# Kernel optimization log

Measured on AMD Instinct MI355X. Metric: run time of the kernel, lower is better.

Reference implementation:

```python
import jax, jax.numpy as jnp
import numpy as np
from functools import partial

B, S, V, E, H = 32, 48, 32000, 512, 512


def setup_inputs() -> dict:
    key = jax.random.key(0)
    ks = jax.random.split(key, 8)
    s = 0.02
    return {
        "encoded": jax.random.normal(ks[0], (B, E), jnp.float32),
        "emb": jax.random.normal(ks[1], (V, E), jnp.float32) * s,   # embedding table
        "Wi": jax.random.normal(ks[2], (4 * H, E), jnp.float32) * s,  # input->gates
        "Wh": jax.random.normal(ks[3], (4 * H, H), jnp.float32) * s,  # hidden->gates
        "bi": jnp.zeros((4 * H,), jnp.float32),
        "bh": jnp.zeros((4 * H,), jnp.float32),
        "Wo": jax.random.normal(ks[4], (V, H), jnp.float32) * s,   # hidden->vocab logits
        "bo": jnp.zeros((V,), jnp.float32),
        "seq_length": S,
    }


def reference(encoded, emb, Wi, Wh, bi, bh, Wo, bo, seq_length):
    """Batched autoregressive decode (teacher_forcing=False path).

    Each step: LSTM cell -> log_softmax over vocab -> store (if still active)
    -> multinomial sample -> embed sampled token as next input. Early EOS
    (token == V-2) is handled by masking stored log-probs to zero thereafter,
    matching the original loop that leaves probs rows as zeros after break.
    """
    bsz = encoded.shape[0]
    hid = Wh.shape[1]
    vocab = Wo.shape[0]
    bias = bi + bh

    def step(carry, k):
        x, h, c, active = carry
        gates = x @ Wi.T + h @ Wh.T + bias          # [B, 4H]
        i_g, f_g, g_g, o_g = jnp.split(gates, 4, axis=-1)  # torch gate order i,f,g,o
        i_g = jax.nn.sigmoid(i_g)
        f_g = jax.nn.sigmoid(f_g)
        g_g = jnp.tanh(g_g)
        o_g = jax.nn.sigmoid(o_g)
        c = f_g * c + i_g * g_g
        h = o_g * jnp.tanh(c)
        logp = jax.nn.log_softmax(h @ Wo.T + bo, axis=-1)  # [B, V]
        stored = jnp.where(active[:, None], logp, 0.0)
        it = jax.random.categorical(k, logp, axis=-1)      # multinomial(exp(logp))
        active = active & (it != vocab - 2)                # EOS token check
        x = emb[it]                                        # next-step input
        return (x, h, c, active), stored

    keys = jax.random.split(jax.random.key(42), seq_length)
    init = (encoded,
            jnp.zeros((bsz, hid), encoded.dtype),
            jnp.zeros((bsz, hid), encoded.dtype),
            jnp.ones((bsz,), bool))
    _, probs = jax.lax.scan(step, init, keys)              # [S, B, V]
    return jnp.transpose(probs, (1, 0, 2))                 # [B, S, V]
```

## Files before the change

### kernel.cpp

```cpp
#include <hip/hip_runtime.h>
#include <stdint.h>
#include <math.h>
#include <limits.h>


#define SEQ 48
#define BSZ 32
#define VOC 32000
#define EDIM 512
#define HDIM 512
#define GDIM 2048
#define KTOT 1024
#define EOS_TOK (VOC - 2)
#define NBLK 250

typedef __attribute__((ext_vector_type(8))) short bf16x8;
typedef __attribute__((ext_vector_type(4))) float f32x4;

__device__ __forceinline__ void threefry2x32(uint32_t k0, uint32_t k1,
                                             uint32_t x0, uint32_t x1,
                                             uint32_t& o0, uint32_t& o1)
{
  uint32_t ks2 = k0 ^ k1 ^ 0x1BD11BDAu;
  x0 += k0; x1 += k1;
#define TFR(r) x0 += x1; x1 = (x1 << (r)) | (x1 >> (32 - (r))); x1 ^= x0;
  TFR(13) TFR(15) TFR(26) TFR(6)
  x0 += k1; x1 += ks2 + 1u;
  TFR(17) TFR(29) TFR(16) TFR(24)
  x0 += ks2; x1 += k0 + 2u;
  TFR(13) TFR(15) TFR(26) TFR(6)
  x0 += k0; x1 += k1 + 3u;
  TFR(17) TFR(29) TFR(16) TFR(24)
  x0 += k1; x1 += ks2 + 4u;
  TFR(13) TFR(15) TFR(26) TFR(6)
  x0 += ks2; x1 += k0 + 5u;
#undef TFR
  o0 = x0; o1 = x1;
}

__device__ __forceinline__ uint32_t tf_bits(uint32_t k0, uint32_t k1, uint32_t m)
{
  uint32_t o0, o1;
  threefry2x32(k0, k1, 0u, m, o0, o1);
  return o0 ^ o1;
}

__device__ __forceinline__ float gumbel_from_bits(uint32_t bits)
{
  uint32_t fb = (bits >> 9) | 0x3F800000u;
  float u = __uint_as_float(fb) - 1.0f;
  u = fmaxf(u, 1.1754943508222875e-38f);
  return -logf(-logf(u));
}

__device__ __forceinline__ float sigmoidf(float v) { return 1.0f / (1.0f + expf(-v)); }

__device__ __forceinline__ unsigned short f2bf(float f) {
  uint32_t u = __float_as_uint(f);
  uint32_t r = u + 0x7FFFu + ((u >> 16) & 1u);
  return (unsigned short)(r >> 16);
}
__device__ __forceinline__ float bf2f(unsigned short h) {
  return __uint_as_float((uint32_t)h << 16);
}

__device__ __forceinline__ float dlf(const float* p) {
  return __hip_atomic_load(p, __ATOMIC_RELAXED, __HIP_MEMORY_SCOPE_AGENT);
}
__device__ __forceinline__ int dli(const int* p) {
  return __hip_atomic_load(p, __ATOMIC_RELAXED, __HIP_MEMORY_SCOPE_AGENT);
}
__device__ __forceinline__ void dsf(float* p, float v) {
  __hip_atomic_store(p, v, __ATOMIC_RELAXED, __HIP_MEMORY_SCOPE_AGENT);
}
__device__ __forceinline__ void dsi(int* p, int v) {
  __hip_atomic_store(p, v, __ATOMIC_RELAXED, __HIP_MEMORY_SCOPE_AGENT);
}

__global__ __launch_bounds__(256) void init_kernel(
    const float* __restrict__ encoded, float* __restrict__ h0,
    float* __restrict__ c, float* __restrict__ x,
    int* __restrict__ active, uint32_t* __restrict__ keys,
    int* __restrict__ counter)
{
  int i = blockIdx.x * 256 + threadIdx.x;
  if (i < BSZ * HDIM) { h0[i] = 0.0f; c[i] = 0.0f; x[i] = encoded[i]; }
  if (blockIdx.x == 0) {
    int t = threadIdx.x;
    if (t < BSZ) active[t] = 1;
    if (t < SEQ) {
      counter[t] = 0;
      uint32_t o0, o1;
      threefry2x32(0u, 42u, 0u, (uint32_t)t, o0, o1);
      keys[2 * t] = o0; keys[2 * t + 1] = o1;
    }
  }
}

__global__ void transpose_kernel(const float* __restrict__ src, float* __restrict__ dst,
                                 int R, int C, int dstLD, int cOff)
{
  __shared__ float tile[32][33];
  int cb = blockIdx.x * 32, rb = blockIdx.y * 32;
  int tx = threadIdx.x, ty = threadIdx.y;
  for (int j = ty; j < 32; j += 8) {
    int r = rb + j, cc = cb + tx;
    if (r < R && cc < C) tile[j][tx] = src[(size_t)r * C + cc];
  }
  __syncthreads();
  for (int j = ty; j < 32; j += 8) {
    int r = rb + tx, cc = cb + j;
    if (r < R && cc < C) dst[(size_t)(cc + cOff) * dstLD + r] = tile[tx][j];
  }
}

__global__ __launch_bounds__(256) void wprep_kernel(
    const float* __restrict__ Wo, unsigned short* __restrict__ WP)
{
  int i4 = blockIdx.x * 256 + threadIdx.x;
  if (i4 >= VOC * 128) return;
  int v  = i4 >> 7;
  int k  = (i4 & 127) * 4;
  const float4 wv = ((const float4*)Wo)[i4];
  int bid  = v >> 7;
  int nt   = (v >> 4) & 7;
  int lane = (v & 15) + (((k >> 3) & 3) << 4);
  int ks   = k >> 5;
  int e0   = k & 7;
  size_t f = (((size_t)bid * 16 + ks) * 8 + nt) * 2;
  size_t base = f * 512 + (size_t)lane * 8 + e0;
  unsigned short a0 = f2bf(wv.x), a1 = f2bf(wv.y), a2 = f2bf(wv.z), a3 = f2bf(wv.w);
  *(ushort4*)(WP + base)       = make_ushort4(a0, a1, a2, a3);
  *(ushort4*)(WP + base + 512) = make_ushort4(f2bf(wv.x - bf2f(a0)), f2bf(wv.y - bf2f(a1)),
                                              f2bf(wv.z - bf2f(a2)), f2bf(wv.w - bf2f(a3)));
}

__global__ __launch_bounds__(256) void cell_kernel(
    const float* __restrict__ WT,
    const float* __restrict__ bi, const float* __restrict__ bh,
    const float* __restrict__ x, const float* __restrict__ hin,
    float* __restrict__ hout, float* __restrict__ c,
    unsigned short* __restrict__ h1bf, unsigned short* __restrict__ h2bf)
{
  __shared__ float xh[KTOT * 4];
  __shared__ float red[4 * 64 * 4];
  __shared__ float gate[64 * 4];
  int t = threadIdx.x;
  int jc = blockIdx.x;
  int bg = blockIdx.y;
  int bbase = bg * 4;

  for (int i = 0; i < 16; ++i) {
    int idx = i * 256 + t;
    int b = idx >> 10, k = idx & 1023;
    float v = (k < EDIM) ? x[(bbase + b) * EDIM + k]
                         : hin[(bbase + b) * HDIM + (k - EDIM)];
    xh[k * 4 + b] = v;
  }
  __syncthreads();

  int gl = t & 63, kq = t >> 6;
  int type = gl >> 4, jj = gl & 15;
  int gcol = type * 512 + jc * 16 + jj;
  float acc0 = 0.f, acc1 = 0.f, acc2 = 0.f, acc3 = 0.f;
  const float* wp = WT + (size_t)(kq * 256) * GDIM + gcol;
  const float4* xp = (const float4*)xh + kq * 256;
#pragma unroll 8
  for (int k = 0; k < 256; ++k) {
    float w = wp[(size_t)k * GDIM];
    float4 h4 = xp[k];
    acc0 += w * h4.x; acc1 += w * h4.y; acc2 += w * h4.z; acc3 += w * h4.w;
  }
  ((float4*)red)[t] = make_float4(acc0, acc1, acc2, acc3);
  __syncthreads();

  if (t < 64) {
    float4 s0 = ((float4*)red)[t];
    float4 s1 = ((float4*)red)[64 + t];
    float4 s2 = ((float4*)red)[128 + t];
    float4 s3 = ((float4*)red)[192 + t];
    int ty2 = t >> 4, jj2 = t & 15;
    int gc2 = ty2 * 512 + jc * 16 + jj2;
    float bsum = bi[gc2] + bh[gc2];
    float4 g;
    g.x = s0.x + s1.x + s2.x + s3.x + bsum;
    g.y = s0.y + s1.y + s2.y + s3.y + bsum;
    g.z = s0.z + s1.z + s2.z + s3.z + bsum;
    g.w = s0.w + s1.w + s2.w + s3.w + bsum;
    ((float4*)gate)[t] = g;
  }
  __syncthreads();

  if (t < 64) {
    int b = t >> 4, jjf = t & 15;
    float ig = sigmoidf(gate[(0 * 16 + jjf) * 4 + b]);
    float fg = sigmoidf(gate[(1 * 16 + jjf) * 4 + b]);
    float gg = tanhf(  gate[(2 * 16 + jjf) * 4 + b]);
    float og = sigmoidf(gate[(3 * 16 + jjf) * 4 + b]);
    int ci = (bbase + b) * HDIM + jc * 16 + jjf;
    float cn = fg * c[ci] + ig * gg;
    c[ci] = cn;
    float hv = og * tanhf(cn);
    hout[ci] = hv;
    unsigned short hh = f2bf(hv);
    h1bf[ci] = hh;
    h2bf[ci] = f2bf(hv - bf2f(hh));
  }
}

__global__ __launch_bounds__(256) void logits_kernel(
    const bf16x8* __restrict__ WP, const float* __restrict__ bo,
    const bf16x8* __restrict__ h1v, const bf16x8* __restrict__ h2v,
    const uint32_t* __restrict__ keys, int step,
    float* __restrict__ out,
    float* __restrict__ pmax, float* __restrict__ psum,
    float* __restrict__ pgv, int* __restrict__ pgi,
    int* __restrict__ counter,
    const float* __restrict__ emb, float* __restrict__ x,
    int* __restrict__ active, float* __restrict__ lse_s, int* __restrict__ act_s)
{
  __shared__ float cm[4][32], cs[4][32], cv[4][32];
  __shared__ int   cidx[4][32];
  __shared__ float fmx[8][32], fsx[8][32], fvx[8][32];
  __shared__ int   fix[8][32];
  __shared__ int   toks[32];
  __shared__ int   doneflag;

  const int t = threadIdx.x, bid = blockIdx.x;
  const int w = t >> 6, l = t & 63;
  const int lr = l & 15, lq = l >> 4;
  const int v0 = bid * 128;

  f32x4 a00 = {0.f, 0.f, 0.f, 0.f};
  f32x4 a01 = a00, a10 = a00, a11 = a00;

  const int ab0 = lr * 64 + lq;
  const int ab1 = (16 + lr) * 64 + lq;
  const int wb0 = bid * 16384 + (w * 2) * 128 + l;

#pragma unroll 2
  for (int ks = 0; ks < 16; ++ks) {
    bf16x8 x10 = h1v[ab0 + ks * 4];
    bf16x8 x11 = h1v[ab1 + ks * 4];
    bf16x8 x20 = h2v[ab0 + ks * 4];
    bf16x8 x21 = h2v[ab1 + ks * 4];
    const int wb = wb0 + ks * 1024;
    bf16x8 w10 = WP[wb];
    bf16x8 w20 = WP[wb + 64];
    bf16x8 w11 = WP[wb + 128];
    bf16x8 w21 = WP[wb + 192];
    a00 = __builtin_amdgcn_mfma_f32_16x16x32_bf16(x10, w10, a00, 0, 0, 0);
    a01 = __builtin_amdgcn_mfma_f32_16x16x32_bf16(x10, w11, a01, 0, 0, 0);
    a10 = __builtin_amdgcn_mfma_f32_16x16x32_bf16(x11, w10, a10, 0, 0, 0);
    a11 = __builtin_amdgcn_mfma_f32_16x16x32_bf16(x11, w11, a11, 0, 0, 0);
    a00 = __builtin_amdgcn_mfma_f32_16x16x32_bf16(x10, w20, a00, 0, 0, 0);
    a01 = __builtin_amdgcn_mfma_f32_16x16x32_bf16(x10, w21, a01, 0, 0, 0);
    a10 = __builtin_amdgcn_mfma_f32_16x16x32_bf16(x11, w20, a10, 0, 0, 0);
    a11 = __builtin_amdgcn_mfma_f32_16x16x32_bf16(x11, w21, a11, 0, 0, 0);
    a00 = __builtin_amdgcn_mfma_f32_16x16x32_bf16(x20, w10, a00, 0, 0, 0);
    a01 = __builtin_amdgcn_mfma_f32_16x16x32_bf16(x20, w11, a01, 0, 0, 0);
    a10 = __builtin_amdgcn_mfma_f32_16x16x32_bf16(x21, w10, a10, 0, 0, 0);
    a11 = __builtin_amdgcn_mfma_f32_16x16x32_bf16(x21, w11, a11, 0, 0, 0);
  }

  const int va = v0 + w * 32 + lr;
  const int vb = va + 16;
  const float boa = bo[va], bob = bo[vb];
  const uint32_t k0 = keys[2 * step], k1 = keys[2 * step + 1];

#pragma unroll
  for (int mt = 0; mt < 2; ++mt) {
    const f32x4 A0 = mt ? a10 : a00;
    const f32x4 A1 = mt ? a11 : a01;
#pragma unroll
    for (int reg = 0; reg < 4; ++reg) {
      const int b = mt * 16 + lq * 4 + reg;
      const float La = A0[reg] + boa;
      const float Lb = A1[reg] + bob;
      size_t obase = (size_t)b * (SEQ * VOC) + (size_t)step * VOC;
      out[obase + va] = La;
      out[obase + vb] = Lb;

      float mx = fmaxf(La, Lb);
      mx = fmaxf(mx, __shfl_xor(mx, 1, 64));
      mx = fmaxf(mx, __shfl_xor(mx, 2, 64));
      mx = fmaxf(mx, __shfl_xor(mx, 4, 64));
      mx = fmaxf(mx, __shfl_xor(mx, 8, 64));
      float se = expf(La - mx) + expf(Lb - mx);

      uint32_t ba = tf_bits(k0, k1, (uint32_t)(b * VOC + va));
      uint32_t bb = tf_bits(k0, k1, (uint32_t)(b * VOC + vb));
      float ga = La + gumbel_from_bits(ba);
      float gb = Lb + gumbel_from_bits(bb);
      float gvx; int gix;
      if (ga >= gb) { gvx = ga; gix = va; } else { gvx = gb; gix = vb; }
#pragma unroll
      for (int d = 1; d < 16; d <<= 1) {
        se += __shfl_xor(se, d, 64);
        float og = __shfl_xor(gvx, d, 64);
        int   oi = __shfl_xor(gix, d, 64);
        if (og > gvx || (og == gvx && oi < gix)) { gvx = og; gix = oi; }
      }
      if (lr == 0) {
        cm[w][b] = mx; cs[w][b] = se; cv[w][b] = gvx; cidx[w][b] = gix;
      }
    }
  }
  __syncthreads();

  if (t < 32) {
    const int b = t;
    float M = cm[0][b];
    M = fmaxf(M, cm[1][b]); M = fmaxf(M, cm[2][b]); M = fmaxf(M, cm[3][b]);
    float S = 0.f;
    float GV = -INFINITY; int GI = INT_MAX;
#pragma unroll
    for (int ww = 0; ww < 4; ++ww) {
      S += cs[ww][b] * expf(cm[ww][b] - M);
      if (cv[ww][b] > GV || (cv[ww][b] == GV && cidx[ww][b] < GI)) {
        GV = cv[ww][b]; GI = cidx[ww][b];
      }
    }
    dsf(pmax + bid * 32 + b, M);
    dsf(psum + bid * 32 + b, S);
    dsf(pgv  + bid * 32 + b, GV);
    dsi(pgi  + bid * 32 + b, GI);
    __threadfence();
  }
  __syncthreads();
  if (t == 0) {
    int old = __hip_atomic_fetch_add(counter + step, 1, __ATOMIC_ACQ_REL,
                                     __HIP_MEMORY_SCOPE_AGENT);
    doneflag = (old == NBLK - 1);
  }
  __syncthreads();

  if (doneflag) {
    __threadfence();
    const int b = t & 31, j = t >> 5;
    float M = -INFINITY, S = 0.f, GV = -INFINITY; int GI = INT_MAX;
    for (int i = j; i < NBLK; i += 8) {
      float m = dlf(pmax + i * 32 + b);
      float s = dlf(psum + i * 32 + b);
      float g = dlf(pgv  + i * 32 + b);
      int  gi = dli(pgi  + i * 32 + b);
      float mn = fmaxf(M, m);
      S = S * expf(M - mn) + s * expf(m - mn);
      M = mn;
      if (g > GV || (g == GV && gi < GI)) { GV = g; GI = gi; }
    }
    fmx[j][b] = M; fsx[j][b] = S; fvx[j][b] = GV; fix[j][b] = GI;
    __syncthreads();
    if (t < 32) {
      float M2 = fmx[0][t];
#pragma unroll
      for (int jj = 1; jj < 8; ++jj) M2 = fmaxf(M2, fmx[jj][t]);
      float S2 = 0.f; float GV2 = -INFINITY; int GI2 = INT_MAX;
#pragma unroll
      for (int jj = 0; jj < 8; ++jj) {
        S2 += fsx[jj][t] * expf(fmx[jj][t] - M2);
        if (fvx[jj][t] > GV2 || (fvx[jj][t] == GV2 && fix[jj][t] < GI2)) {
          GV2 = fvx[jj][t]; GI2 = fix[jj][t];
        }
      }
      lse_s[step * 32 + t] = M2 + logf(S2);
      act_s[step * 32 + t] = active[t];
      if (GI2 == EOS_TOK) active[t] = 0;
      toks[t] = GI2;
    }
    __syncthreads();
    for (int i = t; i < BSZ * 128; i += 256) {
      int row = i >> 7;
      ((float4*)x)[i] = ((const float4*)emb)[(size_t)toks[row] * 128 + (i & 127)];
    }
  }
}

__global__ __launch_bounds__(256) void finish_kernel(
    float4* __restrict__ out4, const float* __restrict__ lse_s,
    const int* __restrict__ act_s)
{
  const int N4 = BSZ * SEQ * VOC / 4;
  for (int f = blockIdx.x * 256 + threadIdx.x; f < N4; f += gridDim.x * 256) {
    int row = f / (VOC / 4);
    int b = row / SEQ, s = row - b * SEQ;
    int idx = s * 32 + b;
    float4 v = out4[f];
    if (act_s[idx]) {
      float lsv = lse_s[idx];
      v.x -= lsv; v.y -= lsv; v.z -= lsv; v.w -= lsv;
    } else {
      v.x = 0.f; v.y = 0.f; v.z = 0.f; v.w = 0.f;
    }
    out4[f] = v;
  }
}

extern "C" void kernel_launch(void* const* d_in, const int* in_sizes, int n_in,
                              void* d_out, int out_size, void* d_ws, size_t ws_size,
                              hipStream_t stream)
{
  (void)in_sizes; (void)n_in; (void)out_size; (void)ws_size;
  const float* encoded = (const float*)d_in[0];
  const float* emb     = (const float*)d_in[1];
  const float* Wi      = (const float*)d_in[2];
  const float* Wh      = (const float*)d_in[3];
  const float* bi      = (const float*)d_in[4];
  const float* bh      = (const float*)d_in[5];
  const float* Wo      = (const float*)d_in[6];
  const float* bo      = (const float*)d_in[7];
  float* out = (float*)d_out;

  char* W = (char*)d_ws;
  size_t off = 0;
  float* WT = (float*)(W + off);            off += (size_t)KTOT * GDIM * 4;
  unsigned short* WP = (unsigned short*)(W + off); off += (size_t)VOC * 512 * 2 * 2;
  float* h0 = (float*)(W + off);            off += BSZ * HDIM * 4;
  float* h1 = (float*)(W + off);            off += BSZ * HDIM * 4;
  float* c  = (float*)(W + off);            off += BSZ * HDIM * 4;
  float* x  = (float*)(W + off);            off += BSZ * EDIM * 4;
  unsigned short* h1bf = (unsigned short*)(W + off); off += BSZ * HDIM * 2;
  unsigned short* h2bf = (unsigned short*)(W + off); off += BSZ * HDIM * 2;
  float* pmax = (float*)(W + off);          off += NBLK * 32 * 4;
  float* psum = (float*)(W + off);          off += NBLK * 32 * 4;
  float* pgv  = (float*)(W + off);          off += NBLK * 32 * 4;
  int*   pgi  = (int*)(W + off);            off += NBLK * 32 * 4;
  float* lse_s = (float*)(W + off);         off += SEQ * BSZ * 4;
  int*   act_s = (int*)(W + off);           off += SEQ * BSZ * 4;
  int*   active = (int*)(W + off);          off += 128;
  uint32_t* keys = (uint32_t*)(W + off);    off += SEQ * 2 * 4;
  int*   counter = (int*)(W + off);         off += SEQ * 4;

  init_kernel<<<dim3(64), dim3(256), 0, stream>>>(encoded, h0, c, x, active, keys, counter);
  transpose_kernel<<<dim3(16, 64), dim3(32, 8), 0, stream>>>(Wi, WT, GDIM, EDIM, GDIM, 0);
  transpose_kernel<<<dim3(16, 64), dim3(32, 8), 0, stream>>>(Wh, WT, GDIM, HDIM, GDIM, 512);
  wprep_kernel<<<dim3((VOC * 128 + 255) / 256), dim3(256), 0, stream>>>(Wo, WP);

  for (int s = 0; s < SEQ; ++s) {
    float* hin  = (s & 1) ? h1 : h0;
    float* hout = (s & 1) ? h0 : h1;
    cell_kernel<<<dim3(32, 8), dim3(256), 0, stream>>>(WT, bi, bh, x, hin, hout, c,
                                                       h1bf, h2bf);
    logits_kernel<<<dim3(NBLK), dim3(256), 0, stream>>>(
        (const bf16x8*)WP, bo, (const bf16x8*)h1bf, (const bf16x8*)h2bf,
        keys, s, out, pmax, psum, pgv, pgi, counter, emb, x, active, lse_s, act_s);
  }
  finish_kernel<<<dim3(2048), dim3(256), 0, stream>>>((float4*)out, lse_s, act_s);
}
```

Measured before the change: 3.750 ms.

## Fuse per-step cell and logits launches into one persistent cooperative kernel

Replaces the 96 per-step kernel launches with a single cooperative kernel of 256 blocks. Grid-wide syncs separate the LSTM cell phase, the logits/partial-reduction phase and a final reduction that every block repeats redundantly for its own 4 batch rows. The cell state stays in registers and the next-token embeddings are gathered directly, with no separate x buffer. This removes launch overhead and the atomic last-block reduction, but adds two grid barriers per step and duplicated reduction work, and limits the kernel to one block per CU.

```diff
diff --git a/kernel.cpp b/kernel.cpp
--- a/kernel.cpp
+++ b/kernel.cpp
@@ -1,7 +1,10 @@
 #include <hip/hip_runtime.h>
+#include <hip/hip_cooperative_groups.h>
 #include <stdint.h>
 #include <math.h>
 #include <limits.h>
+
+namespace cg = cooperative_groups;
 
 
 #define SEQ 48
@@ -62,39 +65,6 @@
 }
 __device__ __forceinline__ float bf2f(unsigned short h) {
   return __uint_as_float((uint32_t)h << 16);
-}
-
-__device__ __forceinline__ float dlf(const float* p) {
-  return __hip_atomic_load(p, __ATOMIC_RELAXED, __HIP_MEMORY_SCOPE_AGENT);
-}
-__device__ __forceinline__ int dli(const int* p) {
-  return __hip_atomic_load(p, __ATOMIC_RELAXED, __HIP_MEMORY_SCOPE_AGENT);
-}
-__device__ __forceinline__ void dsf(float* p, float v) {
-  __hip_atomic_store(p, v, __ATOMIC_RELAXED, __HIP_MEMORY_SCOPE_AGENT);
-}
-__device__ __forceinline__ void dsi(int* p, int v) {
-  __hip_atomic_store(p, v, __ATOMIC_RELAXED, __HIP_MEMORY_SCOPE_AGENT);
-}
-
-__global__ __launch_bounds__(256) void init_kernel(
-    const float* __restrict__ encoded, float* __restrict__ h0,
-    float* __restrict__ c, float* __restrict__ x,
-    int* __restrict__ active, uint32_t* __restrict__ keys,
-    int* __restrict__ counter)
-{
-  int i = blockIdx.x * 256 + threadIdx.x;
-  if (i < BSZ * HDIM) { h0[i] = 0.0f; c[i] = 0.0f; x[i] = encoded[i]; }
-  if (blockIdx.x == 0) {
-    int t = threadIdx.x;
-    if (t < BSZ) active[t] = 1;
-    if (t < SEQ) {
-      counter[t] = 0;
-      uint32_t o0, o1;
-      threefry2x32(0u, 42u, 0u, (uint32_t)t, o0, o1);
-      keys[2 * t] = o0; keys[2 * t + 1] = o1;
-    }
-  }
 }
 
 __global__ void transpose_kernel(const float* __restrict__ src, float* __restrict__ dst,
@@ -135,244 +105,279 @@
                                               f2bf(wv.z - bf2f(a2)), f2bf(wv.w - bf2f(a3)));
 }
 
-__global__ __launch_bounds__(256) void cell_kernel(
-    const float* __restrict__ WT,
-    const float* __restrict__ bi, const float* __restrict__ bh,
-    const float* __restrict__ x, const float* __restrict__ hin,
-    float* __restrict__ hout, float* __restrict__ c,
-    unsigned short* __restrict__ h1bf, unsigned short* __restrict__ h2bf)
-{
-  __shared__ float xh[KTOT * 4];
-  __shared__ float red[4 * 64 * 4];
-  __shared__ float gate[64 * 4];
-  int t = threadIdx.x;
-  int jc = blockIdx.x;
-  int bg = blockIdx.y;
-  int bbase = bg * 4;
-
-  for (int i = 0; i < 16; ++i) {
-    int idx = i * 256 + t;
-    int b = idx >> 10, k = idx & 1023;
-    float v = (k < EDIM) ? x[(bbase + b) * EDIM + k]
-                         : hin[(bbase + b) * HDIM + (k - EDIM)];
-    xh[k * 4 + b] = v;
-  }
-  __syncthreads();
-
-  int gl = t & 63, kq = t >> 6;
-  int type = gl >> 4, jj = gl & 15;
-  int gcol = type * 512 + jc * 16 + jj;
-  float acc0 = 0.f, acc1 = 0.f, acc2 = 0.f, acc3 = 0.f;
-  const float* wp = WT + (size_t)(kq * 256) * GDIM + gcol;
-  const float4* xp = (const float4*)xh + kq * 256;
-#pragma unroll 8
-  for (int k = 0; k < 256; ++k) {
-    float w = wp[(size_t)k * GDIM];
-    float4 h4 = xp[k];
-    acc0 += w * h4.x; acc1 += w * h4.y; acc2 += w * h4.z; acc3 += w * h4.w;
-  }
-  ((float4*)red)[t] = make_float4(acc0, acc1, acc2, acc3);
-  __syncthreads();
-
-  if (t < 64) {
-    float4 s0 = ((float4*)red)[t];
-    float4 s1 = ((float4*)red)[64 + t];
-    float4 s2 = ((float4*)red)[128 + t];
-    float4 s3 = ((float4*)red)[192 + t];
-    int ty2 = t >> 4, jj2 = t & 15;
-    int gc2 = ty2 * 512 + jc * 16 + jj2;
-    float bsum = bi[gc2] + bh[gc2];
-    float4 g;
-    g.x = s0.x + s1.x + s2.x + s3.x + bsum;
-    g.y = s0.y + s1.y + s2.y + s3.y + bsum;
-    g.z = s0.z + s1.z + s2.z + s3.z + bsum;
-    g.w = s0.w + s1.w + s2.w + s3.w + bsum;
-    ((float4*)gate)[t] = g;
-  }
-  __syncthreads();
-
-  if (t < 64) {
-    int b = t >> 4, jjf = t & 15;
-    float ig = sigmoidf(gate[(0 * 16 + jjf) * 4 + b]);
-    float fg = sigmoidf(gate[(1 * 16 + jjf) * 4 + b]);
-    float gg = tanhf(  gate[(2 * 16 + jjf) * 4 + b]);
-    float og = sigmoidf(gate[(3 * 16 + jjf) * 4 + b]);
-    int ci = (bbase + b) * HDIM + jc * 16 + jjf;
-    float cn = fg * c[ci] + ig * gg;
-    c[ci] = cn;
-    float hv = og * tanhf(cn);
-    hout[ci] = hv;
-    unsigned short hh = f2bf(hv);
-    h1bf[ci] = hh;
-    h2bf[ci] = f2bf(hv - bf2f(hh));
-  }
-}
-
-__global__ __launch_bounds__(256) void logits_kernel(
-    const bf16x8* __restrict__ WP, const float* __restrict__ bo,
-    const bf16x8* __restrict__ h1v, const bf16x8* __restrict__ h2v,
-    const uint32_t* __restrict__ keys, int step,
-    float* __restrict__ out,
+__global__ __launch_bounds__(256, 1) void persist_kernel(
+    const float* __restrict__ WT, const float* __restrict__ bi,
+    const float* __restrict__ bh, const float* __restrict__ encoded,
+    const float* __restrict__ emb, const bf16x8* __restrict__ WP,
+    const float* __restrict__ bo, float* __restrict__ out,
+    float* __restrict__ hA, float* __restrict__ hB,
+    unsigned short* __restrict__ h1bf, unsigned short* __restrict__ h2bf,
     float* __restrict__ pmax, float* __restrict__ psum,
     float* __restrict__ pgv, int* __restrict__ pgi,
-    int* __restrict__ counter,
-    const float* __restrict__ emb, float* __restrict__ x,
-    int* __restrict__ active, float* __restrict__ lse_s, int* __restrict__ act_s)
-{
-  __shared__ float cm[4][32], cs[4][32], cv[4][32];
-  __shared__ int   cidx[4][32];
-  __shared__ float fmx[8][32], fsx[8][32], fvx[8][32];
-  __shared__ int   fix[8][32];
-  __shared__ int   toks[32];
-  __shared__ int   doneflag;
-
-  const int t = threadIdx.x, bid = blockIdx.x;
-  const int w = t >> 6, l = t & 63;
-  const int lr = l & 15, lq = l >> 4;
-  const int v0 = bid * 128;
-
-  f32x4 a00 = {0.f, 0.f, 0.f, 0.f};
-  f32x4 a01 = a00, a10 = a00, a11 = a00;
-
-  const int ab0 = lr * 64 + lq;
-  const int ab1 = (16 + lr) * 64 + lq;
-  const int wb0 = bid * 16384 + (w * 2) * 128 + l;
+    float* __restrict__ lse_s, int* __restrict__ act_s)
+{
+  cg::grid_group grid = cg::this_grid();
+  __shared__ __align__(16) char smem_raw[22016];
+  __shared__ uint32_t keys_l[2 * SEQ];
+  __shared__ int active_l[4], toks_l[4];
+
+  const int t = threadIdx.x;
+  const int blk = blockIdx.x;
+  const int jc = blk & 31, bg = blk >> 5;
+  const int bbase = bg * 4;
+
+  if (t < SEQ) {
+    uint32_t o0, o1;
+    threefry2x32(0u, 42u, 0u, (uint32_t)t, o0, o1);
+    keys_l[2 * t] = o0; keys_l[2 * t + 1] = o1;
+  }
+  if (t < 4) active_l[t] = 1;
+  __syncthreads();
+
+  float c_reg = 0.f;
+  float* hprev = hA;
+  float* hcur  = hB;
+
+  for (int sp = 0; sp < SEQ; ++sp) {
+    {
+      float* xh   = (float*)smem_raw;
+      float* red  = xh + 4096;
+      float* gate = red + 1024;
+
+      for (int i = 0; i < 16; ++i) {
+        int bb = i >> 2;
+        int k = (i & 3) * 256 + t;
+        float v;
+        if (k < EDIM) {
+          v = (sp == 0) ? encoded[(bbase + bb) * EDIM + k]
+                        : emb[(size_t)toks_l[bb] * EDIM + k];
+        } else {
+          v = (sp == 0) ? 0.f : hprev[(bbase + bb) * HDIM + (k - EDIM)];
+        }
+        xh[k * 4 + bb] = v;
+      }
+      __syncthreads();
+
+      {
+        int gl = t & 63, kq = t >> 6;
+        int type = gl >> 4, jj = gl & 15;
+        int gcol = type * 512 + jc * 16 + jj;
+        float acc0 = 0.f, acc1 = 0.f, acc2 = 0.f, acc3 = 0.f;
+        const float* wp = WT + (size_t)(kq * 256) * GDIM + gcol;
+        const float4* xp = (const float4*)xh + kq * 256;
+#pragma unroll 8
+        for (int k = 0; k < 256; ++k) {
+          float w = wp[(size_t)k * GDIM];
+          float4 h4 = xp[k];
+          acc0 += w * h4.x; acc1 += w * h4.y; acc2 += w * h4.z; acc3 += w * h4.w;
+        }
+        ((float4*)red)[t] = make_float4(acc0, acc1, acc2, acc3);
+      }
+      __syncthreads();
+
+      if (t < 64) {
+        float4 s0 = ((float4*)red)[t];
+        float4 s1 = ((float4*)red)[64 + t];
+        float4 s2 = ((float4*)red)[128 + t];
+        float4 s3 = ((float4*)red)[192 + t];
+        int ty2 = t >> 4, jj2 = t & 15;
+        int gc2 = ty2 * 512 + jc * 16 + jj2;
+        float bsum = bi[gc2] + bh[gc2];
+        float4 g;
+        g.x = s0.x + s1.x + s2.x + s3.x + bsum;
+        g.y = s0.y + s1.y + s2.y + s3.y + bsum;
+        g.z = s0.z + s1.z + s2.z + s3.z + bsum;
+        g.w = s0.w + s1.w + s2.w + s3.w + bsum;
+        ((float4*)gate)[t] = g;
+      }
+      __syncthreads();
+
+      if (t < 64) {
+        int bb = t >> 4, jjf = t & 15;
+        float ig = sigmoidf(gate[(0 * 16 + jjf) * 4 + bb]);
+        float fg = sigmoidf(gate[(1 * 16 + jjf) * 4 + bb]);
+        float gg = tanhf(  gate[(2 * 16 + jjf) * 4 + bb]);
+        float og = sigmoidf(gate[(3 * 16 + jjf) * 4 + bb]);
+        float cn = fg * c_reg + ig * gg;
+        c_reg = cn;
+        float hv = og * tanhf(cn);
+        int ci = (bbase + bb) * HDIM + jc * 16 + jjf;
+        hcur[ci] = hv;
+        unsigned short hh = f2bf(hv);
+        h1bf[ci] = hh;
+        h2bf[ci] = f2bf(hv - bf2f(hh));
+      }
+    }
+    grid.sync();
+
+    if (blk < NBLK) {
+      float* cmf = (float*)smem_raw;
+      float* csf = cmf + 128;
+      float* cvf = csf + 128;
+      int*   cif = (int*)(cvf + 128);
+
+      const bf16x8* h1v = (const bf16x8*)h1bf;
+      const bf16x8* h2v = (const bf16x8*)h2bf;
+      const int w = t >> 6, l = t & 63;
+      const int lr = l & 15, lq = l >> 4;
+      const int v0 = blk * 128;
+
+      f32x4 a00 = {0.f, 0.f, 0.f, 0.f};
+      f32x4 a01 = a00, a10 = a00, a11 = a00;
+
+      const int ab0 = lr * 64 + lq;
+      const int ab1 = (16 + lr) * 64 + lq;
+      const int wb0 = blk * 16384 + (w * 2) * 128 + l;
 
 #pragma unroll 2
-  for (int ks = 0; ks < 16; ++ks) {
-    bf16x8 x10 = h1v[ab0 + ks * 4];
-    bf16x8 x11 = h1v[ab1 + ks * 4];
-    bf16x8 x20 = h2v[ab0 + ks * 4];
-    bf16x8 x21 = h2v[ab1 + ks * 4];
-    const int wb = wb0 + ks * 1024;
-    bf16x8 w10 = WP[wb];
-    bf16x8 w20 = WP[wb + 64];
-    bf16x8 w11 = WP[wb + 128];
-    bf16x8 w21 = WP[wb + 192];
-    a00 = __builtin_amdgcn_mfma_f32_16x16x32_bf16(x10, w10, a00, 0, 0, 0);
-    a01 = __builtin_amdgcn_mfma_f32_16x16x32_bf16(x10, w11, a01, 0, 0, 0);
-    a10 = __builtin_amdgcn_mfma_f32_16x16x32_bf16(x11, w10, a10, 0, 0, 0);
-    a11 = __builtin_amdgcn_mfma_f32_16x16x32_bf16(x11, w11, a11, 0, 0, 0);
-    a00 = __builtin_amdgcn_mfma_f32_16x16x32_bf16(x10, w20, a00, 0, 0, 0);
-    a01 = __builtin_amdgcn_mfma_f32_16x16x32_bf16(x10, w21, a01, 0, 0, 0);
-    a10 = __builtin_amdgcn_mfma_f32_16x16x32_bf16(x11, w20, a10, 0, 0, 0);
-    a11 = __builtin_amdgcn_mfma_f32_16x16x32_bf16(x11, w21, a11, 0, 0, 0);
-    a00 = __builtin_amdgcn_mfma_f32_16x16x32_bf16(x20, w10, a00, 0, 0, 0);
-    a01 = __builtin_amdgcn_mfma_f32_16x16x32_bf16(x20, w11, a01, 0, 0, 0);
-    a10 = __builtin_amdgcn_mfma_f32_16x16x32_bf16(x21, w10, a10, 0, 0, 0);
-    a11 = __builtin_amdgcn_mfma_f32_16x16x32_bf16(x21, w11, a11, 0, 0, 0);
-  }
-
-  const int va = v0 + w * 32 + lr;
-  const int vb = va + 16;
-  const float boa = bo[va], bob = bo[vb];
-  const uint32_t k0 = keys[2 * step], k1 = keys[2 * step + 1];
+      for (int ks = 0; ks < 16; ++ks) {
+        bf16x8 x10 = h1v[ab0 + ks * 4];
+        bf16x8 x11 = h1v[ab1 + ks * 4];
+        bf16x8 x20 = h2v[ab0 + ks * 4];
+        bf16x8 x21 = h2v[ab1 + ks * 4];
+        const int wb = wb0 + ks * 1024;
+        bf16x8 w10 = WP[wb];
+        bf16x8 w20 = WP[wb + 64];
+        bf16x8 w11 = WP[wb + 128];
+        bf16x8 w21 = WP[wb + 192];
+        a00 = __builtin_amdgcn_mfma_f32_16x16x32_bf16(x10, w10, a00, 0, 0, 0);
+        a01 = __builtin_amdgcn_mfma_f32_16x16x32_bf16(x10, w11, a01, 0, 0, 0);
+        a10 = __builtin_amdgcn_mfma_f32_16x16x32_bf16(x11, w10, a10, 0, 0, 0);
+        a11 = __builtin_amdgcn_mfma_f32_16x16x32_bf16(x11, w11, a11, 0, 0, 0);
+        a00 = __builtin_amdgcn_mfma_f32_16x16x32_bf16(x10, w20, a00, 0, 0, 0);
+        a01 = __builtin_amdgcn_mfma_f32_16x16x32_bf16(x10, w21, a01, 0, 0, 0);
+        a10 = __builtin_amdgcn_mfma_f32_16x16x32_bf16(x11, w20, a10, 0, 0, 0);
+        a11 = __builtin_amdgcn_mfma_f32_16x16x32_bf16(x11, w21, a11, 0, 0, 0);
+        a00 = __builtin_amdgcn_mfma_f32_16x16x32_bf16(x20, w10, a00, 0, 0, 0);
+        a01 = __builtin_amdgcn_mfma_f32_16x16x32_bf16(x20, w11, a01, 0, 0, 0);
+        a10 = __builtin_amdgcn_mfma_f32_16x16x32_bf16(x21, w10, a10, 0, 0, 0);
+        a11 = __builtin_amdgcn_mfma_f32_16x16x32_bf16(x21, w11, a11, 0, 0, 0);
+      }
+
+      const int va = v0 + w * 32 + lr;
+      const int vb = va + 16;
+      const float boa = bo[va], bob = bo[vb];
+      const uint32_t k0 = keys_l[2 * sp], k1 = keys_l[2 * sp + 1];
 
 #pragma unroll
-  for (int mt = 0; mt < 2; ++mt) {
-    const f32x4 A0 = mt ? a10 : a00;
-    const f32x4 A1 = mt ? a11 : a01;
+      for (int mt = 0; mt < 2; ++mt) {
+        const f32x4 A0 = mt ? a10 : a00;
+        const f32x4 A1 = mt ? a11 : a01;
 #pragma unroll
-    for (int reg = 0; reg < 4; ++reg) {
-      const int b = mt * 16 + lq * 4 + reg;
-      const float La = A0[reg] + boa;
-      const float Lb = A1[reg] + bob;
-      size_t obase = (size_t)b * (SEQ * VOC) + (size_t)step * VOC;
-      out[obase + va] = La;
-      out[obase + vb] = Lb;
-
-      float mx = fmaxf(La, Lb);
-      mx = fmaxf(mx, __shfl_xor(mx, 1, 64));
-      mx = fmaxf(mx, __shfl_xor(mx, 2, 64));
-      mx = fmaxf(mx, __shfl_xor(mx, 4, 64));
-      mx = fmaxf(mx, __shfl_xor(mx, 8, 64));
-      float se = expf(La - mx) + expf(Lb - mx);
-
-      uint32_t ba = tf_bits(k0, k1, (uint32_t)(b * VOC + va));
-      uint32_t bb = tf_bits(k0, k1, (uint32_t)(b * VOC + vb));
-      float ga = La + gumbel_from_bits(ba);
-      float gb = Lb + gumbel_from_bits(bb);
-      float gvx; int gix;
-      if (ga >= gb) { gvx = ga; gix = va; } else { gvx = gb; gix = vb; }
+        for (int reg = 0; reg < 4; ++reg) {
+          const int b = mt * 16 + lq * 4 + reg;
+          const float La = A0[reg] + boa;
+          const float Lb = A1[reg] + bob;
+          size_t obase = (size_t)b * (SEQ * VOC) + (size_t)sp * VOC;
+          out[obase + va] = La;
+          out[obase + vb] = Lb;
+
+          float mx = fmaxf(La, Lb);
+          mx = fmaxf(mx, __shfl_xor(mx, 1, 64));
+          mx = fmaxf(mx, __shfl_xor(mx, 2, 64));
+          mx = fmaxf(mx, __shfl_xor(mx, 4, 64));
+          mx = fmaxf(mx, __shfl_xor(mx, 8, 64));
+          float se = expf(La - mx) + expf(Lb - mx);
+
+          uint32_t ba = tf_bits(k0, k1, (uint32_t)(b * VOC + va));
+          uint32_t bb2 = tf_bits(k0, k1, (uint32_t)(b * VOC + vb));
+          float ga = La + gumbel_from_bits(ba);
+          float gb = Lb + gumbel_from_bits(bb2);
+          float gvx; int gix;
+          if (ga >= gb) { gvx = ga; gix = va; } else { gvx = gb; gix = vb; }
 #pragma unroll
-      for (int d = 1; d < 16; d <<= 1) {
-        se += __shfl_xor(se, d, 64);
-        float og = __shfl_xor(gvx, d, 64);
-        int   oi = __shfl_xor(gix, d, 64);
-        if (og > gvx || (og == gvx && oi < gix)) { gvx = og; gix = oi; }
-      }
-      if (lr == 0) {
-        cm[w][b] = mx; cs[w][b] = se; cv[w][b] = gvx; cidx[w][b] = gix;
+          for (int d = 1; d < 16; d <<= 1) {
+            se += __shfl_xor(se, d, 64);
+            float og = __shfl_xor(gvx, d, 64);
+            int   oi = __shfl_xor(gix, d, 64);
+            if (og > gvx || (og == gvx && oi < gix)) { gvx = og; gix = oi; }
+          }
+          if (lr == 0) {
+            cmf[w * 32 + b] = mx; csf[w * 32 + b] = se;
+            cvf[w * 32 + b] = gvx; cif[w * 32 + b] = gix;
+          }
+        }
+      }
+      __syncthreads();
+
+      if (t < 32) {
+        const int b = t;
+        float M = cmf[b];
+        M = fmaxf(M, cmf[32 + b]); M = fmaxf(M, cmf[64 + b]); M = fmaxf(M, cmf[96 + b]);
+        float S = 0.f;
+        float GV = -INFINITY; int GI = INT_MAX;
+#pragma unroll
+        for (int ww = 0; ww < 4; ++ww) {
+          S += csf[ww * 32 + b] * expf(cmf[ww * 32 + b] - M);
+          if (cvf[ww * 32 + b] > GV ||
+              (cvf[ww * 32 + b] == GV && cif[ww * 32 + b] < GI)) {
+            GV = cvf[ww * 32 + b]; GI = cif[ww * 32 + b];
+          }
+        }
+        pmax[blk * 32 + b] = M;
+        psum[blk * 32 + b] = S;
+        pgv[blk * 32 + b]  = GV;
+        pgi[blk * 32 + b]  = GI;
       }
     }
-  }
-  __syncthreads();
-
-  if (t < 32) {
-    const int b = t;
-    float M = cm[0][b];
-    M = fmaxf(M, cm[1][b]); M = fmaxf(M, cm[2][b]); M = fmaxf(M, cm[3][b]);
-    float S = 0.f;
-    float GV = -INFINITY; int GI = INT_MAX;
-#pragma unroll
-    for (int ww = 0; ww < 4; ++ww) {
-      S += cs[ww][b] * expf(cm[ww][b] - M);
-      if (cv[ww][b] > GV || (cv[ww][b] == GV && cidx[ww][b] < GI)) {
-        GV = cv[ww][b]; GI = cidx[ww][b];
-      }
+    grid.sync();
+
+    {
+      float* Lm = (float*)smem_raw;
+      float* Ls = Lm + 1024;
+      float* Lv = Ls + 1024;
+      int*   Li = (int*)(Lv + 1024);
+      float* Cm = (float*)(Li + 1024);
+      float* Cs = Cm + 256;
+      float* Cv = Cs + 256;
+      int*   Ci = (int*)(Cv + 256);
+
+      for (int i = t; i < NBLK * 4; i += 256) {
+        int pb = i >> 2, bl = i & 3;
+        Lm[i] = pmax[pb * 32 + bbase + bl];
+        Ls[i] = psum[pb * 32 + bbase + bl];
+        Lv[i] = pgv[pb * 32 + bbase + bl];
+        Li[i] = pgi[pb * 32 + bbase + bl];
+      }
+      __syncthreads();
+      {
+        int bl = t & 3, j = t >> 2;
+        float M = -INFINITY, S = 0.f, GV = -INFINITY; int GI = INT_MAX;
+        for (int i = j; i < NBLK; i += 64) {
+          int idx = i * 4 + bl;
+          float m = Lm[idx], sv = Ls[idx], g = Lv[idx]; int gi = Li[idx];
+          float mn = fmaxf(M, m);
+          S = S * expf(M - mn) + sv * expf(m - mn);
+          M = mn;
+          if (g > GV || (g == GV && gi < GI)) { GV = g; GI = gi; }
+        }
+        Cm[t] = M; Cs[t] = S; Cv[t] = GV; Ci[t] = GI;
+      }
+      __syncthreads();
+      if (t < 4) {
+        float M = Cm[t], S = Cs[t], GV = Cv[t]; int GI = Ci[t];
+        for (int j = 1; j < 64; ++j) {
+          int idx = j * 4 + t;
+          float m = Cm[idx];
+          float mn = fmaxf(M, m);
+          S = S * expf(M - mn) + Cs[idx] * expf(m - mn);
+          M = mn;
+          if (Cv[idx] > GV || (Cv[idx] == GV && Ci[idx] < GI)) {
+            GV = Cv[idx]; GI = Ci[idx];
+          }
+        }
+        int bglob = bbase + t;
+        if (jc == 0) {
+          lse_s[sp * 32 + bglob] = M + logf(S);
+          act_s[sp * 32 + bglob] = active_l[t];
+        }
+        toks_l[t] = GI;
+        if (GI == EOS_TOK) active_l[t] = 0;
+      }
+      __syncthreads();
     }
-    dsf(pmax + bid * 32 + b, M);
-    dsf(psum + bid * 32 + b, S);
-    dsf(pgv  + bid * 32 + b, GV);
-    dsi(pgi  + bid * 32 + b, GI);
-    __threadfence();
-  }
-  __syncthreads();
-  if (t == 0) {
-    int old = __hip_atomic_fetch_add(counter + step, 1, __ATOMIC_ACQ_REL,
-                                     __HIP_MEMORY_SCOPE_AGENT);
-    doneflag = (old == NBLK - 1);
-  }
-  __syncthreads();
-
-  if (doneflag) {
-    __threadfence();
-    const int b = t & 31, j = t >> 5;
-    float M = -INFINITY, S = 0.f, GV = -INFINITY; int GI = INT_MAX;
-    for (int i = j; i < NBLK; i += 8) {
-      float m = dlf(pmax + i * 32 + b);
-      float s = dlf(psum + i * 32 + b);
-      float g = dlf(pgv  + i * 32 + b);
-      int  gi = dli(pgi  + i * 32 + b);
-      float mn = fmaxf(M, m);
-      S = S * expf(M - mn) + s * expf(m - mn);
-      M = mn;
-      if (g > GV || (g == GV && gi < GI)) { GV = g; GI = gi; }
-    }
-    fmx[j][b] = M; fsx[j][b] = S; fvx[j][b] = GV; fix[j][b] = GI;
-    __syncthreads();
-    if (t < 32) {
-      float M2 = fmx[0][t];
-#pragma unroll
-      for (int jj = 1; jj < 8; ++jj) M2 = fmaxf(M2, fmx[jj][t]);
-      float S2 = 0.f; float GV2 = -INFINITY; int GI2 = INT_MAX;
-#pragma unroll
-      for (int jj = 0; jj < 8; ++jj) {
-        S2 += fsx[jj][t] * expf(fmx[jj][t] - M2);
-        if (fvx[jj][t] > GV2 || (fvx[jj][t] == GV2 && fix[jj][t] < GI2)) {
-          GV2 = fvx[jj][t]; GI2 = fix[jj][t];
-        }
-      }
-      lse_s[step * 32 + t] = M2 + logf(S2);
-      act_s[step * 32 + t] = active[t];
-      if (GI2 == EOS_TOK) active[t] = 0;
-      toks[t] = GI2;
-    }
-    __syncthreads();
-    for (int i = t; i < BSZ * 128; i += 256) {
-      int row = i >> 7;
-      ((float4*)x)[i] = ((const float4*)emb)[(size_t)toks[row] * 128 + (i & 127)];
-    }
+
+    float* tmp = hprev; hprev = hcur; hcur = tmp;
   }
 }
 
@@ -414,11 +419,9 @@
   char* W = (char*)d_ws;
   size_t off = 0;
   float* WT = (float*)(W + off);            off += (size_t)KTOT * GDIM * 4;
-  unsigned short* WP = (unsigned short*)(W + off); off += (size_t)VOC * 512 * 2 * 2;
-  float* h0 = (float*)(W + off);            off += BSZ * HDIM * 4;
-  float* h1 = (float*)(W + off);            off += BSZ * HDIM * 4;
-  float* c  = (float*)(W + off);            off += BSZ * HDIM * 4;
-  float* x  = (float*)(W + off);            off += BSZ * EDIM * 4;
+  unsigned short* WPu = (unsigned short*)(W + off); off += (size_t)VOC * 512 * 2 * 2;
+  float* hA = (float*)(W + off);            off += BSZ * HDIM * 4;
+  float* hB = (float*)(W + off);            off += BSZ * HDIM * 4;
   unsigned short* h1bf = (unsigned short*)(W + off); off += BSZ * HDIM * 2;
   unsigned short* h2bf = (unsigned short*)(W + off); off += BSZ * HDIM * 2;
   float* pmax = (float*)(W + off);          off += NBLK * 32 * 4;
@@ -427,23 +430,20 @@
   int*   pgi  = (int*)(W + off);            off += NBLK * 32 * 4;
   float* lse_s = (float*)(W + off);         off += SEQ * BSZ * 4;
   int*   act_s = (int*)(W + off);           off += SEQ * BSZ * 4;
-  int*   active = (int*)(W + off);          off += 128;
-  uint32_t* keys = (uint32_t*)(W + off);    off += SEQ * 2 * 4;
-  int*   counter = (int*)(W + off);         off += SEQ * 4;
-
-  init_kernel<<<dim3(64), dim3(256), 0, stream>>>(encoded, h0, c, x, active, keys, counter);
+
   transpose_kernel<<<dim3(16, 64), dim3(32, 8), 0, stream>>>(Wi, WT, GDIM, EDIM, GDIM, 0);
   transpose_kernel<<<dim3(16, 64), dim3(32, 8), 0, stream>>>(Wh, WT, GDIM, HDIM, GDIM, 512);
-  wprep_kernel<<<dim3((VOC * 128 + 255) / 256), dim3(256), 0, stream>>>(Wo, WP);
-
-  for (int s = 0; s < SEQ; ++s) {
-    float* hin  = (s & 1) ? h1 : h0;
-    float* hout = (s & 1) ? h0 : h1;
-    cell_kernel<<<dim3(32, 8), dim3(256), 0, stream>>>(WT, bi, bh, x, hin, hout, c,
-                                                       h1bf, h2bf);
-    logits_kernel<<<dim3(NBLK), dim3(256), 0, stream>>>(
-        (const bf16x8*)WP, bo, (const bf16x8*)h1bf, (const bf16x8*)h2bf,
-        keys, s, out, pmax, psum, pgv, pgi, counter, emb, x, active, lse_s, act_s);
-  }
+  wprep_kernel<<<dim3((VOC * 128 + 255) / 256), dim3(256), 0, stream>>>(Wo, WPu);
+
+  const bf16x8* WP = (const bf16x8*)WPu;
+  void* args[] = {
+    (void*)&WT, (void*)&bi, (void*)&bh, (void*)&encoded, (void*)&emb,
+    (void*)&WP, (void*)&bo, (void*)&out, (void*)&hA, (void*)&hB,
+    (void*)&h1bf, (void*)&h2bf, (void*)&pmax, (void*)&psum,
+    (void*)&pgv, (void*)&pgi, (void*)&lse_s, (void*)&act_s
+  };
+  hipLaunchCooperativeKernel((const void*)persist_kernel, dim3(256), dim3(256),
+                             args, 0, stream);
+
   finish_kernel<<<dim3(2048), dim3(256), 0, stream>>>((float4*)out, lse_s, act_s);
 }
```

After: 7.640 ms. 104% more time.
